# Kernel tuning notes

Hardware: AMD Instinct MI355X
Metric: run time of the kernel (lower is better)

## Reference

```python
import jax, jax.numpy as jnp
import numpy as np

D_MODEL = 256
D_INNER = 512   # expand=2
D_STATE = 16
D_CONV = 4
DT_RANK = 16    # ceil(256/16)
N_LAYERS = 4
CITY = 300
BATCH = 32
EPS = 1e-5


def setup_inputs() -> dict:
    key = jax.random.key(0)
    ks = jax.random.split(key, 12)
    def rn(k, shape, scale=0.02):
        return (jax.random.normal(k, shape) * scale).astype(jnp.float32)
    inp = {}
    inp["coords"]   = jax.random.uniform(ks[0], (BATCH, CITY, 2), jnp.float32)
    inp["emb_W"]    = rn(ks[1], (D_MODEL, 2), 0.5)
    inp["emb_b"]    = jnp.zeros((D_MODEL,), jnp.float32)
    inp["ln_w"]     = jnp.ones((N_LAYERS, D_MODEL), jnp.float32)
    inp["ln_b"]     = jnp.zeros((N_LAYERS, D_MODEL), jnp.float32)
    inp["in_W"]     = rn(ks[2], (N_LAYERS, 2 * D_INNER, D_MODEL))
    inp["conv_W"]   = rn(ks[3], (N_LAYERS, D_INNER, D_CONV), 0.1)
    inp["conv_b"]   = jnp.zeros((N_LAYERS, D_INNER), jnp.float32)
    inp["xproj_W"]  = rn(ks[4], (N_LAYERS, DT_RANK + 2 * D_STATE, D_INNER))
    inp["dtproj_W"] = rn(ks[5], (N_LAYERS, D_INNER, DT_RANK), 0.1)
    inp["dtproj_b"] = rn(ks[6], (N_LAYERS, D_INNER), 0.1)
    # A initialized like mamba: S4D-real, A = -exp(A_log) with A in [1, 16]
    inp["A_log"]    = jnp.log(1.0 + jax.random.uniform(ks[7], (N_LAYERS, D_INNER, D_STATE), jnp.float32) * 15.0)
    inp["D_skip"]   = jnp.ones((N_LAYERS, D_INNER), jnp.float32)
    inp["out_W"]    = rn(ks[8], (N_LAYERS, D_MODEL, D_INNER))
    inp["normf_w"]  = jnp.ones((D_MODEL,), jnp.float32)
    inp["normf_b"]  = jnp.zeros((D_MODEL,), jnp.float32)
    inp["head_W"]   = rn(ks[9], (CITY, D_MODEL))
    return inp


def _layernorm(x, w, b):
    m = jnp.mean(x, axis=-1, keepdims=True)
    v = jnp.mean(jnp.square(x - m), axis=-1, keepdims=True)
    return (x - m) * jax.lax.rsqrt(v + EPS) * w + b


def _mamba_mixer(x, in_W, conv_W, conv_b, xproj_W, dtproj_W, dtproj_b, A_log, D_skip, out_W):
    # x: (B, L, d_model)
    Bsz = x.shape[0]
    xz = jnp.einsum('bld,ed->ble', x, in_W)            # (B, L, 2*d_inner)
    xi, z = jnp.split(xz, 2, axis=-1)                   # each (B, L, d_inner)
    # causal depthwise conv1d along L
    xc = jnp.swapaxes(xi, 1, 2)                         # (B, d_inner, L)
    xc = jax.lax.conv_general_dilated(
        xc, conv_W[:, None, :], (1,), [(D_CONV - 1, 0)],
        feature_group_count=D_INNER, dimension_numbers=('NCH', 'OIH', 'NCH'))
    xc = jax.nn.silu(jnp.swapaxes(xc, 1, 2) + conv_b)   # (B, L, d_inner)
    dbl = jnp.einsum('bld,ed->ble', xc, xproj_W)        # (B, L, dt_rank + 2*d_state)
    dt, Bm, Cm = jnp.split(dbl, [DT_RANK, DT_RANK + D_STATE], axis=-1)
    dt = jax.nn.softplus(jnp.einsum('blr,dr->bld', dt, dtproj_W) + dtproj_b)  # (B, L, d_inner)
    A = -jnp.exp(A_log)                                 # (d_inner, d_state)

    def step(h, inp):
        x_t, dt_t, B_t, C_t = inp                       # (B,dI),(B,dI),(B,dS),(B,dS)
        dA = jnp.exp(dt_t[..., None] * A)               # (B, dI, dS)
        h = dA * h + (dt_t * x_t)[..., None] * B_t[:, None, :]
        y = jnp.einsum('bds,bs->bd', h, C_t)
        return h, y

    h0 = jnp.zeros((Bsz, D_INNER, D_STATE), x.dtype)
    xs = (jnp.swapaxes(xc, 0, 1), jnp.swapaxes(dt, 0, 1),
          jnp.swapaxes(Bm, 0, 1), jnp.swapaxes(Cm, 0, 1))
    _, ys = jax.lax.scan(step, h0, xs)                  # ys: (L, B, d_inner)
    y = jnp.swapaxes(ys, 0, 1) + xc * D_skip
    y = y * jax.nn.silu(z)
    return jnp.einsum('ble,de->bld', y, out_W)          # (B, L, d_model)


def reference(coords, emb_W, emb_b, ln_w, ln_b, in_W, conv_W, conv_b, xproj_W,
              dtproj_W, dtproj_b, A_log, D_skip, out_W, normf_w, normf_b, head_W):
    x = jnp.einsum('blc,dc->bld', coords, emb_W) + emb_b
    residual = None
    for i in range(N_LAYERS):
        residual = x if residual is None else x + residual
        h = _layernorm(residual, ln_w[i], ln_b[i])
        x = _mamba_mixer(h, in_W[i], conv_W[i], conv_b[i], xproj_W[i],
                         dtproj_W[i], dtproj_b[i], A_log[i], D_skip[i], out_W[i])
    res = x + residual
    # final fused add + RMSNorm (is_rms_norm=True with LayerNorm weight/bias)
    rms = res * jax.lax.rsqrt(jnp.mean(res * res, axis=-1, keepdims=True) + EPS)
    out = rms * normf_w + normf_b
    logits = jnp.einsum('bld,cd->blc', out, head_W)     # (B, L, city_count)
    return logits
```

## Files before the change

kernel.cpp:

```cpp
#include <hip/hip_runtime.h>
#include <hip/hip_bf16.h>
#include <math.h>

#define D_MODEL 256
#define D_INNER 512
#define D_STATE 16
#define D_CONV 4
#define DT_RANK 16
#define N_LAYERS 4
#define CITY 300
#define BATCH 32
#define SEQ 300
#define NTOK (BATCH * SEQ)
#define NSEG 15
#define SEGLEN (SEQ / NSEG)

typedef __attribute__((ext_vector_type(8))) short short8v;
typedef __attribute__((ext_vector_type(4))) float f32x4;
typedef __attribute__((ext_vector_type(2))) float f32x2;

#define L2E_F 1.44269504088896340736f
#define LN2_F 0.69314718055994530942f

__device__ __forceinline__ float fexp2(float x) { return __builtin_amdgcn_exp2f(x); }
__device__ __forceinline__ float flog2(float x) { return __builtin_amdgcn_logf(x); }

__device__ __forceinline__ float fast_sig(float x) {
    return __builtin_amdgcn_rcpf(1.f + fexp2(-x * L2E_F));
}

__device__ __forceinline__ float softplus_f(float x) {
    float t = fexp2(-fabsf(x) * L2E_F);
    return fmaxf(x, 0.f) + flog2(1.f + t) * LN2_F;
}

__device__ __forceinline__ unsigned short f2b(float a) {
    __hip_bfloat16 h = __float2bfloat16(a);
    return *reinterpret_cast<unsigned short*>(&h);
}

__device__ __forceinline__ float b2f(unsigned short u) {
    unsigned int x = ((unsigned int)u) << 16;
    return __uint_as_float(x);
}

__device__ __forceinline__ float dtproj8(const float* rb, const f32x2* w2, float dtbv) {
    const f32x2* r2 = (const f32x2*)rb;
    f32x2 a0, a1, a2, a3;
    a0.x = dtbv; a0.y = 0.f;
    a1.x = 0.f; a1.y = 0.f;
    a2 = a1; a3 = a1;
    a0 = __builtin_elementwise_fma(r2[0], w2[0], a0);
    a1 = __builtin_elementwise_fma(r2[1], w2[1], a1);
    a2 = __builtin_elementwise_fma(r2[2], w2[2], a2);
    a3 = __builtin_elementwise_fma(r2[3], w2[3], a3);
    a0 = __builtin_elementwise_fma(r2[4], w2[4], a0);
    a1 = __builtin_elementwise_fma(r2[5], w2[5], a1);
    a2 = __builtin_elementwise_fma(r2[6], w2[6], a2);
    a3 = __builtin_elementwise_fma(r2[7], w2[7], a3);
    f32x2 s = (a0 + a1) + (a2 + a3);
    return s.x + s.y;
}

__global__ void cvt4_kernel(const float* __restrict__ s0, unsigned short* __restrict__ d0, int n0,
                            const float* __restrict__ s1, unsigned short* __restrict__ d1, int n1,
                            const float* __restrict__ s2, unsigned short* __restrict__ d2, int n2,
                            const float* __restrict__ s3, unsigned short* __restrict__ d3, int n3) {
    int stride = gridDim.x * blockDim.x;
    int tid = blockIdx.x * blockDim.x + threadIdx.x;
    for (int i = tid; i < n0 / 4; i += stride) {
        float4 v = ((const float4*)s0)[i];
        ushort4 o; o.x = f2b(v.x); o.y = f2b(v.y); o.z = f2b(v.z); o.w = f2b(v.w);
        ((ushort4*)d0)[i] = o;
    }
    for (int i = tid; i < n1 / 4; i += stride) {
        float4 v = ((const float4*)s1)[i];
        ushort4 o; o.x = f2b(v.x); o.y = f2b(v.y); o.z = f2b(v.z); o.w = f2b(v.w);
        ((ushort4*)d1)[i] = o;
    }
    for (int i = tid; i < n2 / 4; i += stride) {
        float4 v = ((const float4*)s2)[i];
        ushort4 o; o.x = f2b(v.x); o.y = f2b(v.y); o.z = f2b(v.z); o.w = f2b(v.w);
        ((ushort4*)d2)[i] = o;
    }
    for (int i = tid; i < n3 / 4; i += stride) {
        float4 v = ((const float4*)s3)[i];
        ushort4 o; o.x = f2b(v.x); o.y = f2b(v.y); o.z = f2b(v.z); o.w = f2b(v.w);
        ((ushort4*)d3)[i] = o;
    }
}

__global__ void embed_ln_kernel(const float* __restrict__ coords,
                                const float* __restrict__ eW,
                                const float* __restrict__ eb,
                                const float* __restrict__ w,
                                const float* __restrict__ b,
                                float* __restrict__ resid,
                                unsigned short* __restrict__ hb) {
    int t = blockIdx.x, d = threadIdx.x;
    float c0 = coords[t * 2 + 0];
    float c1 = coords[t * 2 + 1];
    float r = c0 * eW[d * 2 + 0] + c1 * eW[d * 2 + 1] + eb[d];
    resid[t * D_MODEL + d] = r;
    float s1 = r, s2 = r * r;
#pragma unroll
    for (int m = 1; m < 64; m <<= 1) {
        s1 += __shfl_xor(s1, m);
        s2 += __shfl_xor(s2, m);
    }
    __shared__ float p1[4], p2[4];
    if ((d & 63) == 0) { p1[d >> 6] = s1; p2[d >> 6] = s2; }
    __syncthreads();
    s1 = (p1[0] + p1[1]) + (p1[2] + p1[3]);
    s2 = (p2[0] + p2[1]) + (p2[2] + p2[3]);
    float mean = s1 * (1.f / D_MODEL);
    float var = s2 * (1.f / D_MODEL) - mean * mean;
    hb[t * D_MODEL + d] = f2b((r - mean) * rsqrtf(var + 1e-5f) * w[d] + b[d]);
}

template <int BM, int BN, bool GN, bool OB>
__global__ __launch_bounds__(256, 2) void gemm_mfma(const unsigned short* __restrict__ A,
                                                    const unsigned short* __restrict__ W,
                                                    void* __restrict__ C, int N, int K) {
    constexpr int TI = BM / 32;
    constexpr int TJ = BN / 32;
    __shared__ short Als[BM * 32];
    __shared__ short Bls[BN * 32];
    const int tid = threadIdx.x;
    const int lane = tid & 63, wid = tid >> 6;
    const int wr = wid >> 1, wc = wid & 1;
    const int t0 = blockIdx.x * BM, n0 = blockIdx.y * BN;
    f32x4 acc[TI][TJ] = {};

    for (int k0 = 0; k0 < K; k0 += 32) {
#pragma unroll
        for (int it = 0; it < BM / 64; ++it) {
            int s = tid + it * 256;
            int m = s >> 2, q = s & 3;
            uint4 p = *(const uint4*)(A + (size_t)(t0 + m) * K + k0 + q * 8);
            *(uint4*)&Als[(((m >> 4) * 4 + q) * 16 + (m & 15)) * 8] = p;
        }
#pragma unroll
        for (int it = 0; it < BN / 64; ++it) {
            int s = tid + it * 256;
            int n = s >> 2, q = s & 3;
            int nrow = n0 + n;
            uint4 p = make_uint4(0u, 0u, 0u, 0u);
            if (!GN || nrow < N)
                p = *(const uint4*)(W + (size_t)nrow * K + k0 + q * 8);
            *(uint4*)&Bls[(((n >> 4) * 4 + q) * 16 + (n & 15)) * 8] = p;
        }
        __syncthreads();
        short8v af[TI], bf[TJ];
#pragma unroll
        for (int i = 0; i < TI; i++)
            af[i] = *(const short8v*)&Als[(wr * TI + i) * 512 + lane * 8];
#pragma unroll
        for (int j = 0; j < TJ; j++)
            bf[j] = *(const short8v*)&Bls[(wc * TJ + j) * 512 + lane * 8];
#pragma unroll
        for (int i = 0; i < TI; i++)
#pragma unroll
            for (int j = 0; j < TJ; j++)
                acc[i][j] = __builtin_amdgcn_mfma_f32_16x16x32_bf16(
                    af[i], bf[j], acc[i][j], 0, 0, 0);
        __syncthreads();
    }
    const int rq = lane >> 4, cn = lane & 15;
#pragma unroll
    for (int i = 0; i < TI; i++) {
        int trow = t0 + wr * (BM / 2) + i * 16 + rq * 4;
#pragma unroll
        for (int j = 0; j < TJ; j++) {
            int ncol = n0 + wc * (BN / 2) + j * 16 + cn;
            if (!GN || ncol < N) {
#pragma unroll
                for (int reg = 0; reg < 4; reg++) {
                    if constexpr (OB)
                        ((unsigned short*)C)[(size_t)(trow + reg) * N + ncol] =
                            f2b(acc[i][j][reg]);
                    else
                        ((float*)C)[(size_t)(trow + reg) * N + ncol] = acc[i][j][reg];
                }
            }
        }
    }
}

__global__ __launch_bounds__(256, 2) void xproj_conv(
    const unsigned short* __restrict__ xzb,
    const float* __restrict__ cW, const float* __restrict__ cb,
    const unsigned short* __restrict__ W,
    unsigned short* __restrict__ xcb, float* __restrict__ dblo) {
    constexpr int TI = 2, TJ = 2;
    const int K = D_INNER, N = 48;
    __shared__ short Als[64 * 32];
    __shared__ short Bls[64 * 32];
    __shared__ float cwL[D_INNER * 4];
    __shared__ float cbL[D_INNER];
    const int tid = threadIdx.x;
    const int lane = tid & 63, wid = tid >> 6;
    const int wr = wid >> 1, wc = wid & 1;
    const int t0 = blockIdx.x * 64;

    for (int i = tid; i < D_INNER; i += 256) {
        ((float4*)cwL)[i] = ((const float4*)cW)[i];
        cbL[i] = cb[i];
    }
    __syncthreads();

    f32x4 acc[TI][TJ] = {};
    const int m = tid >> 2, q = tid & 3;
    const int t = t0 + m;
    const int l = t % SEQ;

    for (int k0 = 0; k0 < K; k0 += 32) {
        {
            const int ch0 = k0 + q * 8;
            const unsigned short* xr = xzb + (size_t)t * 1024 + ch0;
            uint4 u0 = make_uint4(0u, 0u, 0u, 0u), u1 = u0, u2 = u0, u3;
            if (l >= 3) u0 = *(const uint4*)(xr - 3 * 1024);
            if (l >= 2) u1 = *(const uint4*)(xr - 2 * 1024);
            if (l >= 1) u2 = *(const uint4*)(xr - 1 * 1024);
            u3 = *(const uint4*)xr;
            unsigned int ow0, ow1, ow2, ow3;
#pragma unroll
            for (int c2 = 0; c2 < 4; c2++) {
                unsigned int w0 = (c2 == 0) ? u0.x : (c2 == 1) ? u0.y : (c2 == 2) ? u0.z : u0.w;
                unsigned int w1 = (c2 == 0) ? u1.x : (c2 == 1) ? u1.y : (c2 == 2) ? u1.z : u1.w;
                unsigned int w2 = (c2 == 0) ? u2.x : (c2 == 1) ? u2.y : (c2 == 2) ? u2.z : u2.w;
                unsigned int w3 = (c2 == 0) ? u3.x : (c2 == 1) ? u3.y : (c2 == 2) ? u3.z : u3.w;
                int chA = ch0 + c2 * 2, chB = chA + 1;
                float4 wvA = *(const float4*)&cwL[chA * 4];
                float4 wvB = *(const float4*)&cwL[chB * 4];
                float aA = cbL[chA], aB = cbL[chB];
                aA = fmaf(b2f((unsigned short)(w0 & 0xffffu)), wvA.x, aA);
                aB = fmaf(b2f((unsigned short)(w0 >> 16)), wvB.x, aB);
                aA = fmaf(b2f((unsigned short)(w1 & 0xffffu)), wvA.y, aA);
                aB = fmaf(b2f((unsigned short)(w1 >> 16)), wvB.y, aB);
                aA = fmaf(b2f((unsigned short)(w2 & 0xffffu)), wvA.z, aA);
                aB = fmaf(b2f((unsigned short)(w2 >> 16)), wvB.z, aB);
                aA = fmaf(b2f((unsigned short)(w3 & 0xffffu)), wvA.w, aA);
                aB = fmaf(b2f((unsigned short)(w3 >> 16)), wvB.w, aB);
                aA = aA * fast_sig(aA);
                aB = aB * fast_sig(aB);
                unsigned int pk = (unsigned int)f2b(aA) | ((unsigned int)f2b(aB) << 16);
                if (c2 == 0) ow0 = pk; else if (c2 == 1) ow1 = pk; else if (c2 == 2) ow2 = pk; else ow3 = pk;
            }
            uint4 pk4 = make_uint4(ow0, ow1, ow2, ow3);
            *(uint4*)&Als[(((m >> 4) * 4 + q) * 16 + (m & 15)) * 8] = pk4;
            *(uint4*)(xcb + (size_t)t * 512 + ch0) = pk4;
        }
        {
            int n = tid >> 2;
            uint4 p = make_uint4(0u, 0u, 0u, 0u);
            if (n < N) p = *(const uint4*)(W + (size_t)n * K + k0 + q * 8);
            *(uint4*)&Bls[(((n >> 4) * 4 + q) * 16 + (n & 15)) * 8] = p;
        }
        __syncthreads();
        short8v af[TI], bf[TJ];
#pragma unroll
        for (int i = 0; i < TI; i++)
            af[i] = *(const short8v*)&Als[(wr * TI + i) * 512 + lane * 8];
#pragma unroll
        for (int j = 0; j < TJ; j++)
            bf[j] = *(const short8v*)&Bls[(wc * TJ + j) * 512 + lane * 8];
#pragma unroll
        for (int i = 0; i < TI; i++)
#pragma unroll
            for (int j = 0; j < TJ; j++)
                acc[i][j] = __builtin_amdgcn_mfma_f32_16x16x32_bf16(
                    af[i], bf[j], acc[i][j], 0, 0, 0);
        __syncthreads();
    }
    const int rq = lane >> 4, cn = lane & 15;
#pragma unroll
    for (int i = 0; i < TI; i++) {
        int trow = t0 + (wr * TI + i) * 16 + rq * 4;
#pragma unroll
        for (int j = 0; j < TJ; j++) {
            int ncol = wc * 32 + j * 16 + cn;
            if (ncol < N) {
#pragma unroll
                for (int reg = 0; reg < 4; reg++)
                    dblo[(size_t)(trow + reg) * N + ncol] = acc[i][j][reg];
            }
        }
    }
}

template <bool RMS, bool HEAD>
__global__ __launch_bounds__(256, 2) void gemm_out_ln(const unsigned short* __restrict__ A,
                                                      const unsigned short* __restrict__ W,
                                                      float* __restrict__ resid,
                                                      const float* __restrict__ w,
                                                      const float* __restrict__ b,
                                                      unsigned short* __restrict__ hb,
                                                      const unsigned short* __restrict__ hW,
                                                      float* __restrict__ outp) {
    constexpr int TI = 2, TJ = 8;
    const int K = D_INNER;
    __shared__ short Als[64 * 32];
    __shared__ short Bls[256 * 32];
    __shared__ float rs1[2][64], rs2[2][64];
    __shared__ short hN[HEAD ? 64 * 256 : 1];
    const int tid = threadIdx.x;
    const int lane = tid & 63, wid = tid >> 6;
    const int wr = wid >> 1, wc = wid & 1;
    const int t0 = blockIdx.x * 64;
    f32x4 acc[TI][TJ] = {};

    for (int k0 = 0; k0 < K; k0 += 32) {
        {
            int s = tid;
            int m = s >> 2, q = s & 3;
            uint4 p = *(const uint4*)(A + (size_t)(t0 + m) * K + k0 + q * 8);
            *(uint4*)&Als[(((m >> 4) * 4 + q) * 16 + (m & 15)) * 8] = p;
        }
#pragma unroll
        for (int it = 0; it < 4; ++it) {
            int s = tid + it * 256;
            int n = s >> 2, q = s & 3;
            uint4 p = *(const uint4*)(W + (size_t)n * K + k0 + q * 8);
            *(uint4*)&Bls[(((n >> 4) * 4 + q) * 16 + (n & 15)) * 8] = p;
        }
        __syncthreads();
        short8v af[TI], bf[TJ];
#pragma unroll
        for (int i = 0; i < TI; i++)
            af[i] = *(const short8v*)&Als[(wr * TI + i) * 512 + lane * 8];
#pragma unroll
        for (int j = 0; j < TJ; j++)
            bf[j] = *(const short8v*)&Bls[(wc * TJ + j) * 512 + lane * 8];
#pragma unroll
        for (int i = 0; i < TI; i++)
#pragma unroll
            for (int j = 0; j < TJ; j++)
                acc[i][j] = __builtin_amdgcn_mfma_f32_16x16x32_bf16(
                    af[i], bf[j], acc[i][j], 0, 0, 0);
        __syncthreads();
    }
    const int rq = lane >> 4, cn = lane & 15;
    float s1p[TI][4], s2p[TI][4];
#pragma unroll
    for (int i = 0; i < TI; i++) {
        int trow = t0 + wr * 32 + i * 16 + rq * 4;
#pragma unroll
        for (int reg = 0; reg < 4; reg++) { s1p[i][reg] = 0.f; s2p[i][reg] = 0.f; }
#pragma unroll
        for (int j = 0; j < TJ; j++) {
            int c = wc * 128 + j * 16 + cn;
#pragma unroll
            for (int reg = 0; reg < 4; reg++) {
                float rv = acc[i][j][reg] + resid[(size_t)(trow + reg) * D_MODEL + c];
                acc[i][j][reg] = rv;
                s1p[i][reg] += rv;
                s2p[i][reg] = fmaf(rv, rv, s2p[i][reg]);
            }
        }
    }
#pragma unroll
    for (int m = 1; m < 16; m <<= 1) {
#pragma unroll
        for (int i = 0; i < TI; i++)
#pragma unroll
            for (int reg = 0; reg < 4; reg++) {
                s1p[i][reg] += __shfl_xor(s1p[i][reg], m);
                s2p[i][reg] += __shfl_xor(s2p[i][reg], m);
            }
    }
    if (cn == 0) {
#pragma unroll
        for (int i = 0; i < TI; i++)
#pragma unroll
            for (int reg = 0; reg < 4; reg++) {
                int rloc = wr * 32 + i * 16 + rq * 4 + reg;
                rs1[wc][rloc] = s1p[i][reg];
                rs2[wc][rloc] = s2p[i][reg];
            }
    }
    __syncthreads();
    float wv[TJ], bv[TJ];
#pragma unroll
    for (int j = 0; j < TJ; j++) {
        int c = wc * 128 + j * 16 + cn;
        wv[j] = w[c];
        bv[j] = b[c];
    }
#pragma unroll
    for (int i = 0; i < TI; i++) {
        int trow = t0 + wr * 32 + i * 16 + rq * 4;
#pragma unroll
        for (int reg = 0; reg < 4; reg++) {
            int rloc = wr * 32 + i * 16 + rq * 4 + reg;
            float S1 = rs1[0][rloc] + rs1[1][rloc];
            float S2 = rs2[0][rloc] + rs2[1][rloc];
            float mean, rstd;
            if constexpr (RMS) {
                mean = 0.f;
                rstd = rsqrtf(S2 * (1.f / D_MODEL) + 1e-5f);
            } else {
                mean = S1 * (1.f / D_MODEL);
                float var = S2 * (1.f / D_MODEL) - mean * mean;
                rstd = rsqrtf(var + 1e-5f);
            }
#pragma unroll
            for (int j = 0; j < TJ; j++) {
                int c = wc * 128 + j * 16 + cn;
                float rv = acc[i][j][reg];
                unsigned short nv = f2b((rv - mean) * rstd * wv[j] + bv[j]);
                if constexpr (HEAD) {
                    int mrow = wr * 32 + i * 16 + rq * 4 + reg;
                    hN[(c >> 5) * 2048 + (((mrow >> 4) * 4 + ((c & 31) >> 3)) * 16 + (mrow & 15)) * 8 + (c & 7)] = (short)nv;
                } else {
                    hb[(size_t)(trow + reg) * D_MODEL + c] = nv;
                }
                if constexpr (!RMS)
                    resid[(size_t)(trow + reg) * D_MODEL + c] = rv;
            }
        }
    }
    if constexpr (HEAD) {
        __syncthreads();
        for (int nch = 0; nch < 5; ++nch) {
            f32x4 acc2[2][2] = {};
            for (int k0 = 0; k0 < D_MODEL; k0 += 32) {
                int n = tid >> 2, q = tid & 3;
                int nrow = nch * 64 + n;
                uint4 p = make_uint4(0u, 0u, 0u, 0u);
                if (nrow < CITY) p = *(const uint4*)(hW + (size_t)nrow * D_MODEL + k0 + q * 8);
                *(uint4*)&Bls[(((n >> 4) * 4 + q) * 16 + (n & 15)) * 8] = p;
                __syncthreads();
                short8v af2[2], bf2[2];
#pragma unroll
                for (int i = 0; i < 2; i++)
                    af2[i] = *(const short8v*)&hN[(k0 >> 5) * 2048 + (wr * 2 + i) * 512 + lane * 8];
#pragma unroll
                for (int j = 0; j < 2; j++)
                    bf2[j] = *(const short8v*)&Bls[(wc * 2 + j) * 512 + lane * 8];
#pragma unroll
                for (int i = 0; i < 2; i++)
#pragma unroll
                    for (int j = 0; j < 2; j++)
                        acc2[i][j] = __builtin_amdgcn_mfma_f32_16x16x32_bf16(
                            af2[i], bf2[j], acc2[i][j], 0, 0, 0);
                __syncthreads();
            }
#pragma unroll
            for (int i = 0; i < 2; i++) {
                int trow = t0 + (wr * 2 + i) * 16 + rq * 4;
#pragma unroll
                for (int j = 0; j < 2; j++) {
                    int ncol = nch * 64 + wc * 32 + j * 16 + cn;
                    if (ncol < CITY) {
#pragma unroll
                        for (int reg = 0; reg < 4; reg++)
                            outp[(size_t)(trow + reg) * CITY + ncol] = acc2[i][j][reg];
                    }
                }
            }
        }
    }
}

__global__ __launch_bounds__(960) void scan_block(
    const unsigned short* __restrict__ xcb, const float* __restrict__ dbl,
    const unsigned short* __restrict__ xzb,
    const float* __restrict__ A_log, const float* __restrict__ Dskip,
    const float* __restrict__ dtW, const float* __restrict__ dtb,
    float* __restrict__ dts, unsigned short* __restrict__ yb) {
    __shared__ float lh[NSEG * D_STATE * 64];
    __shared__ float lsd[NSEG * 64];
    const int b = blockIdx.x, dg = blockIdx.y;
    const int tid = threadIdx.x;
    const int lane = tid & 63;
    const int seg = __builtin_amdgcn_readfirstlane(tid >> 6);
    const int d = (dg << 6) + lane;
    f32x2 A2[8], w2[8];
#pragma unroll
    for (int s4 = 0; s4 < 4; s4++) {
        float4 v = *(const float4*)(A_log + (size_t)d * D_STATE + s4 * 4);
        f32x2 pa, pb;
        pa.x = -fexp2(v.x * L2E_F) * L2E_F;
        pa.y = -fexp2(v.y * L2E_F) * L2E_F;
        pb.x = -fexp2(v.z * L2E_F) * L2E_F;
        pb.y = -fexp2(v.w * L2E_F) * L2E_F;
        A2[s4 * 2 + 0] = pa;
        A2[s4 * 2 + 1] = pb;
        float4 w = *(const float4*)(dtW + (size_t)d * DT_RANK + s4 * 4);
        f32x2 qa, qb;
        qa.x = w.x; qa.y = w.y;
        qb.x = w.z; qb.y = w.w;
        w2[s4 * 2 + 0] = qa;
        w2[s4 * 2 + 1] = qb;
    }
    const float dtbv = dtb[d], dsk = Dskip[d];
    const size_t tb = (size_t)b * SEQ + (size_t)seg * SEGLEN;
    const float* __restrict__ dr = dbl + tb * 48;
    const unsigned short* __restrict__ xp = xcb + tb * 512 + d;
    const unsigned short* __restrict__ zp = xzb + tb * 1024 + 512 + d;
    float* __restrict__ dtp = dts + tb * 512 + d;
    unsigned short* __restrict__ yp = yb + tb * 512 + d;

    {
        f32x2 h2[8];
#pragma unroll
        for (int i = 0; i < 8; i++) { h2[i].x = 0.f; h2[i].y = 0.f; }
        float sdt = 0.f;
        float dbA[32], dbB[32];
#pragma unroll
        for (int i = 0; i < 8; i++) ((float4*)dbA)[i] = ((const float4*)dr)[i];
        float xv = b2f(xp[0]);
        for (int l = 0; l < SEGLEN; l += 2) {
            const float4* nr1 = (const float4*)(dr + (size_t)(l + 1) * 48);
#pragma unroll
            for (int i = 0; i < 8; i++) ((float4*)dbB)[i] = nr1[i];
            float xv1 = b2f(xp[(size_t)(l + 1) * 512]);
            {
                float acc = dtproj8(dbA, w2, dtbv);
                float dtt = softplus_f(acc);
                dtp[(size_t)l * 512] = dtt;
                sdt += dtt;
                float dtx = dtt * xv;
                f32x2 dtt2, dtx2;
                dtt2.x = dtt; dtt2.y = dtt;
                dtx2.x = dtx; dtx2.y = dtx;
                const f32x2* B2 = (const f32x2*)(dbA + 16);
#pragma unroll
                for (int i = 0; i < 8; i++) {
                    f32x2 g = dtt2 * A2[i];
                    f32x2 e;
                    e.x = fexp2(g.x);
                    e.y = fexp2(g.y);
                    h2[i] = __builtin_elementwise_fma(e, h2[i], dtx2 * B2[i]);
                }
            }
            const float4* nr2 = (const float4*)(dr + (size_t)(l + 2) * 48);
#pragma unroll
            for (int i = 0; i < 8; i++) ((float4*)dbA)[i] = nr2[i];
            float xv2 = b2f(xp[(size_t)(l + 2) * 512]);
            if (l + 1 < SEGLEN) {
                float acc = dtproj8(dbB, w2, dtbv);
                float dtt = softplus_f(acc);
                dtp[(size_t)(l + 1) * 512] = dtt;
                sdt += dtt;
                float dtx = dtt * xv1;
                f32x2 dtt2, dtx2;
                dtt2.x = dtt; dtt2.y = dtt;
                dtx2.x = dtx; dtx2.y = dtx;
                const f32x2* B2 = (const f32x2*)(dbB + 16);
#pragma unroll
                for (int i = 0; i < 8; i++) {
                    f32x2 g = dtt2 * A2[i];
                    f32x2 e;
                    e.x = fexp2(g.x);
                    e.y = fexp2(g.y);
                    h2[i] = __builtin_elementwise_fma(e, h2[i], dtx2 * B2[i]);
                }
            }
            xv = xv2;
        }
#pragma unroll
        for (int i = 0; i < 8; i++) {
            lh[(seg * D_STATE + 2 * i + 0) * 64 + lane] = h2[i].x;
            lh[(seg * D_STATE + 2 * i + 1) * 64 + lane] = h2[i].y;
        }
        lsd[seg * 64 + lane] = sdt;
    }
    __syncthreads();
    for (int it = tid; it < D_STATE * 64; it += 960) {
        int ch = it & 63, s = it >> 6;
        float As2 = -fexp2(A_log[(size_t)((dg << 6) + ch) * D_STATE + s] * L2E_F) * L2E_F;
        float hl[NSEG], sd[NSEG];
#pragma unroll
        for (int sg = 0; sg < NSEG; sg++) {
            hl[sg] = lh[(sg * D_STATE + s) * 64 + ch];
            sd[sg] = lsd[sg * 64 + ch];
        }
        float H = 0.f;
#pragma unroll
        for (int sg = 0; sg < NSEG; sg++) {
            lh[(sg * D_STATE + s) * 64 + ch] = H;
            H = fmaf(fexp2(As2 * sd[sg]), H, hl[sg]);
        }
    }
    __syncthreads();
    {
        f32x2 h2[8];
#pragma unroll
        for (int i = 0; i < 8; i++) {
            h2[i].x = lh[(seg * D_STATE + 2 * i + 0) * 64 + lane];
            h2[i].y = lh[(seg * D_STATE + 2 * i + 1) * 64 + lane];
        }
        float dbA[32], dbB[32];
#pragma unroll
        for (int i = 0; i < 8; i++) ((float4*)dbA)[i] = ((const float4*)(dr + 16))[i];
        float xv = b2f(xp[0]), zv = b2f(zp[0]);
        float dt0 = dtp[0];
        for (int l = 0; l < SEGLEN; l += 2) {
            const float4* nr1 = (const float4*)(dr + (size_t)(l + 1) * 48 + 16);
#pragma unroll
            for (int i = 0; i < 8; i++) ((float4*)dbB)[i] = nr1[i];
            float xv1 = b2f(xp[(size_t)(l + 1) * 512]);
            float zv1 = b2f(zp[(size_t)(l + 1) * 1024]);
            float dt1 = dtp[(size_t)(l + 1) * 512];
            {
                float dtt = dt0;
                float dtx = dtt * xv;
                f32x2 dtt2, dtx2;
                dtt2.x = dtt; dtt2.y = dtt;
                dtx2.x = dtx; dtx2.y = dtx;
                f32x2 ya, yc;
                ya.x = 0.f; ya.y = 0.f; yc = ya;
                const f32x2* B2 = (const f32x2*)dbA;
                const f32x2* C2 = (const f32x2*)(dbA + 16);
#pragma unroll
                for (int i = 0; i < 8; i++) {
                    f32x2 g = dtt2 * A2[i];
                    f32x2 e;
                    e.x = fexp2(g.x);
                    e.y = fexp2(g.y);
                    h2[i] = __builtin_elementwise_fma(e, h2[i], dtx2 * B2[i]);
                    if (i & 1)
                        yc = __builtin_elementwise_fma(h2[i], C2[i], yc);
                    else
                        ya = __builtin_elementwise_fma(h2[i], C2[i], ya);
                }
                f32x2 ys = ya + yc;
                float y = ys.x + ys.y;
                yp[(size_t)l * 512] = f2b((y + xv * dsk) * (zv * fast_sig(zv)));
            }
            const float4* nr2 = (const float4*)(dr + (size_t)(l + 2) * 48 + 16);
#pragma unroll
            for (int i = 0; i < 8; i++) ((float4*)dbA)[i] = nr2[i];
            float xv2 = b2f(xp[(size_t)(l + 2) * 512]);
            float zv2 = b2f(zp[(size_t)(l + 2) * 1024]);
            float dt2 = dtp[(size_t)(l + 2) * 512];
            if (l + 1 < SEGLEN) {
                float dtt = dt1;
                float dtx = dtt * xv1;
                f32x2 dtt2, dtx2;
                dtt2.x = dtt; dtt2.y = dtt;
                dtx2.x = dtx; dtx2.y = dtx;
                f32x2 ya, yc;
                ya.x = 0.f; ya.y = 0.f; yc = ya;
                const f32x2* B2 = (const f32x2*)dbB;
                const f32x2* C2 = (const f32x2*)(dbB + 16);
#pragma unroll
                for (int i = 0; i < 8; i++) {
                    f32x2 g = dtt2 * A2[i];
                    f32x2 e;
                    e.x = fexp2(g.x);
                    e.y = fexp2(g.y);
                    h2[i] = __builtin_elementwise_fma(e, h2[i], dtx2 * B2[i]);
                    if (i & 1)
                        yc = __builtin_elementwise_fma(h2[i], C2[i], yc);
                    else
                        ya = __builtin_elementwise_fma(h2[i], C2[i], ya);
                }
                f32x2 ys = ya + yc;
                float y = ys.x + ys.y;
                yp[(size_t)(l + 1) * 512] = f2b((y + xv1 * dsk) * (zv1 * fast_sig(zv1)));
            }
            xv = xv2; zv = zv2; dt0 = dt2;
        }
    }
}

extern "C" void kernel_launch(void* const* d_in, const int* in_sizes, int n_in,
                              void* d_out, int out_size, void* d_ws, size_t ws_size,
                              hipStream_t stream) {
    const float* coords   = (const float*)d_in[0];
    const float* emb_W    = (const float*)d_in[1];
    const float* emb_b    = (const float*)d_in[2];
    const float* ln_w     = (const float*)d_in[3];
    const float* ln_b     = (const float*)d_in[4];
    const float* in_W     = (const float*)d_in[5];
    const float* conv_W   = (const float*)d_in[6];
    const float* conv_b   = (const float*)d_in[7];
    const float* xproj_W  = (const float*)d_in[8];
    const float* dtproj_W = (const float*)d_in[9];
    const float* dtproj_b = (const float*)d_in[10];
    const float* A_log    = (const float*)d_in[11];
    const float* D_skip   = (const float*)d_in[12];
    const float* out_W    = (const float*)d_in[13];
    const float* normf_w  = (const float*)d_in[14];
    const float* normf_b  = (const float*)d_in[15];
    const float* head_W   = (const float*)d_in[16];
    float* out = (float*)d_out;

    const int T = NTOK;
    float* resid = (float*)d_ws;
    float* dbl   = resid + (size_t)T * D_MODEL;
    float* dts   = dbl + (size_t)T * 48;
    unsigned short* hb     = (unsigned short*)(dts + (size_t)T * D_INNER);
    unsigned short* xzb    = hb + (size_t)T * D_MODEL;
    unsigned short* xcb    = xzb + (size_t)T * 2 * D_INNER;
    unsigned short* yb     = xcb + (size_t)T * D_INNER;
    unsigned short* wb_in  = yb + (size_t)T * D_INNER;
    unsigned short* wb_xp  = wb_in + (size_t)N_LAYERS * 2 * D_INNER * D_MODEL;
    unsigned short* wb_out = wb_xp + (size_t)N_LAYERS * 48 * D_INNER;
    unsigned short* wb_hd  = wb_out + (size_t)N_LAYERS * D_MODEL * D_INNER;

    cvt4_kernel<<<256, 256, 0, stream>>>(
        in_W, wb_in, N_LAYERS * 2 * D_INNER * D_MODEL,
        xproj_W, wb_xp, N_LAYERS * 48 * D_INNER,
        out_W, wb_out, N_LAYERS * D_MODEL * D_INNER,
        head_W, wb_hd, CITY * D_MODEL);

    embed_ln_kernel<<<T, D_MODEL, 0, stream>>>(coords, emb_W, emb_b, ln_w, ln_b, resid, hb);

    for (int i = 0; i < N_LAYERS; i++) {
        gemm_mfma<128, 128, false, true><<<dim3(T / 128, 8), 256, 0, stream>>>(
            hb, wb_in + (size_t)i * 2 * D_INNER * D_MODEL, xzb, 2 * D_INNER, D_MODEL);
        xproj_conv<<<T / 64, 256, 0, stream>>>(
            xzb, conv_W + i * D_INNER * D_CONV, conv_b + i * D_INNER,
            wb_xp + (size_t)i * 48 * D_INNER, xcb, dbl);
        scan_block<<<dim3(BATCH, 8), 960, 0, stream>>>(
            xcb, dbl, xzb, A_log + (size_t)i * D_INNER * D_STATE, D_skip + i * D_INNER,
            dtproj_W + (size_t)i * D_INNER * DT_RANK, dtproj_b + i * D_INNER, dts, yb);
        if (i < N_LAYERS - 1)
            gemm_out_ln<false, false><<<T / 64, 256, 0, stream>>>(
                yb, wb_out + (size_t)i * D_MODEL * D_INNER, resid,
                ln_w + (i + 1) * D_MODEL, ln_b + (i + 1) * D_MODEL, hb, nullptr, nullptr);
        else
            gemm_out_ln<true, true><<<T / 64, 256, 0, stream>>>(
                yb, wb_out + (size_t)i * D_MODEL * D_INNER, resid,
                normf_w, normf_b, hb, wb_hd, out);
    }
}
```

Baseline: 463.2 us.

## Compute local scan output in first pass, correct with carried-in state in second

The chunked scan now computes the full local output (zero-initial-state contribution plus D skip) during the first pass and writes it to a new fp32 workspace buffer. The second pass then only propagates the carried-in prefix state, which decays by exp(dt*A) and is dotted with C, then adds it to the stored partial before gating. This removes the B*x update and dt/x reloads from the second pass, shortening the work after the segment-combine barrier. In exchange it adds an extra fp32 write and read per element and more register pressure from 48-float row buffers in the first pass.

```diff
diff --git a/kernel.cpp b/kernel.cpp
--- a/kernel.cpp
+++ b/kernel.cpp
@@ -468,7 +468,8 @@
     const unsigned short* __restrict__ xzb,
     const float* __restrict__ A_log, const float* __restrict__ Dskip,
     const float* __restrict__ dtW, const float* __restrict__ dtb,
-    float* __restrict__ dts, unsigned short* __restrict__ yb) {
+    float* __restrict__ dts, float* __restrict__ wls,
+    unsigned short* __restrict__ yb) {
     __shared__ float lh[NSEG * D_STATE * 64];
     __shared__ float lsd[NSEG * 64];
     const int b = blockIdx.x, dg = blockIdx.y;
@@ -500,6 +501,7 @@
     const unsigned short* __restrict__ xp = xcb + tb * 512 + d;
     const unsigned short* __restrict__ zp = xzb + tb * 1024 + 512 + d;
     float* __restrict__ dtp = dts + tb * 512 + d;
+    float* __restrict__ wlp = wls + tb * 512 + d;
     unsigned short* __restrict__ yp = yb + tb * 512 + d;
 
     {
@@ -507,14 +509,14 @@
 #pragma unroll
         for (int i = 0; i < 8; i++) { h2[i].x = 0.f; h2[i].y = 0.f; }
         float sdt = 0.f;
-        float dbA[32], dbB[32];
-#pragma unroll
-        for (int i = 0; i < 8; i++) ((float4*)dbA)[i] = ((const float4*)dr)[i];
+        float dbA[48], dbB[48];
+#pragma unroll
+        for (int i = 0; i < 12; i++) ((float4*)dbA)[i] = ((const float4*)dr)[i];
         float xv = b2f(xp[0]);
         for (int l = 0; l < SEGLEN; l += 2) {
             const float4* nr1 = (const float4*)(dr + (size_t)(l + 1) * 48);
 #pragma unroll
-            for (int i = 0; i < 8; i++) ((float4*)dbB)[i] = nr1[i];
+            for (int i = 0; i < 12; i++) ((float4*)dbB)[i] = nr1[i];
             float xv1 = b2f(xp[(size_t)(l + 1) * 512]);
             {
                 float acc = dtproj8(dbA, w2, dtbv);
@@ -526,94 +528,9 @@
                 dtt2.x = dtt; dtt2.y = dtt;
                 dtx2.x = dtx; dtx2.y = dtx;
                 const f32x2* B2 = (const f32x2*)(dbA + 16);
-#pragma unroll
-                for (int i = 0; i < 8; i++) {
-                    f32x2 g = dtt2 * A2[i];
-                    f32x2 e;
-                    e.x = fexp2(g.x);
-                    e.y = fexp2(g.y);
-                    h2[i] = __builtin_elementwise_fma(e, h2[i], dtx2 * B2[i]);
-                }
-            }
-            const float4* nr2 = (const float4*)(dr + (size_t)(l + 2) * 48);
-#pragma unroll
-            for (int i = 0; i < 8; i++) ((float4*)dbA)[i] = nr2[i];
-            float xv2 = b2f(xp[(size_t)(l + 2) * 512]);
-            if (l + 1 < SEGLEN) {
-                float acc = dtproj8(dbB, w2, dtbv);
-                float dtt = softplus_f(acc);
-                dtp[(size_t)(l + 1) * 512] = dtt;
-                sdt += dtt;
-                float dtx = dtt * xv1;
-                f32x2 dtt2, dtx2;
-                dtt2.x = dtt; dtt2.y = dtt;
-                dtx2.x = dtx; dtx2.y = dtx;
-                const f32x2* B2 = (const f32x2*)(dbB + 16);
-#pragma unroll
-                for (int i = 0; i < 8; i++) {
-                    f32x2 g = dtt2 * A2[i];
-                    f32x2 e;
-                    e.x = fexp2(g.x);
-                    e.y = fexp2(g.y);
-                    h2[i] = __builtin_elementwise_fma(e, h2[i], dtx2 * B2[i]);
-                }
-            }
-            xv = xv2;
-        }
-#pragma unroll
-        for (int i = 0; i < 8; i++) {
-            lh[(seg * D_STATE + 2 * i + 0) * 64 + lane] = h2[i].x;
-            lh[(seg * D_STATE + 2 * i + 1) * 64 + lane] = h2[i].y;
-        }
-        lsd[seg * 64 + lane] = sdt;
-    }
-    __syncthreads();
-    for (int it = tid; it < D_STATE * 64; it += 960) {
-        int ch = it & 63, s = it >> 6;
-        float As2 = -fexp2(A_log[(size_t)((dg << 6) + ch) * D_STATE + s] * L2E_F) * L2E_F;
-        float hl[NSEG], sd[NSEG];
-#pragma unroll
-        for (int sg = 0; sg < NSEG; sg++) {
-            hl[sg] = lh[(sg * D_STATE + s) * 64 + ch];
-            sd[sg] = lsd[sg * 64 + ch];
-        }
-        float H = 0.f;
-#pragma unroll
-        for (int sg = 0; sg < NSEG; sg++) {
-            lh[(sg * D_STATE + s) * 64 + ch] = H;
-            H = fmaf(fexp2(As2 * sd[sg]), H, hl[sg]);
-        }
-    }
-    __syncthreads();
-    {
-        f32x2 h2[8];
-#pragma unroll
-        for (int i = 0; i < 8; i++) {
-            h2[i].x = lh[(seg * D_STATE + 2 * i + 0) * 64 + lane];
-            h2[i].y = lh[(seg * D_STATE + 2 * i + 1) * 64 + lane];
-        }
-        float dbA[32], dbB[32];
-#pragma unroll
-        for (int i = 0; i < 8; i++) ((float4*)dbA)[i] = ((const float4*)(dr + 16))[i];
-        float xv = b2f(xp[0]), zv = b2f(zp[0]);
-        float dt0 = dtp[0];
-        for (int l = 0; l < SEGLEN; l += 2) {
-            const float4* nr1 = (const float4*)(dr + (size_t)(l + 1) * 48 + 16);
-#pragma unroll
-            for (int i = 0; i < 8; i++) ((float4*)dbB)[i] = nr1[i];
-            float xv1 = b2f(xp[(size_t)(l + 1) * 512]);
-            float zv1 = b2f(zp[(size_t)(l + 1) * 1024]);
-            float dt1 = dtp[(size_t)(l + 1) * 512];
-            {
-                float dtt = dt0;
-                float dtx = dtt * xv;
-                f32x2 dtt2, dtx2;
-                dtt2.x = dtt; dtt2.y = dtt;
-                dtx2.x = dtx; dtx2.y = dtx;
+                const f32x2* C2 = (const f32x2*)(dbA + 32);
                 f32x2 ya, yc;
                 ya.x = 0.f; ya.y = 0.f; yc = ya;
-                const f32x2* B2 = (const f32x2*)dbA;
-                const f32x2* C2 = (const f32x2*)(dbA + 16);
 #pragma unroll
                 for (int i = 0; i < 8; i++) {
                     f32x2 g = dtt2 * A2[i];
@@ -627,25 +544,25 @@
                         ya = __builtin_elementwise_fma(h2[i], C2[i], ya);
                 }
                 f32x2 ys = ya + yc;
-                float y = ys.x + ys.y;
-                yp[(size_t)l * 512] = f2b((y + xv * dsk) * (zv * fast_sig(zv)));
-            }
-            const float4* nr2 = (const float4*)(dr + (size_t)(l + 2) * 48 + 16);
-#pragma unroll
-            for (int i = 0; i < 8; i++) ((float4*)dbA)[i] = nr2[i];
+                wlp[(size_t)l * 512] = (ys.x + ys.y) + xv * dsk;
+            }
+            const float4* nr2 = (const float4*)(dr + (size_t)(l + 2) * 48);
+#pragma unroll
+            for (int i = 0; i < 12; i++) ((float4*)dbA)[i] = nr2[i];
             float xv2 = b2f(xp[(size_t)(l + 2) * 512]);
-            float zv2 = b2f(zp[(size_t)(l + 2) * 1024]);
-            float dt2 = dtp[(size_t)(l + 2) * 512];
             if (l + 1 < SEGLEN) {
-                float dtt = dt1;
+                float acc = dtproj8(dbB, w2, dtbv);
+                float dtt = softplus_f(acc);
+                dtp[(size_t)(l + 1) * 512] = dtt;
+                sdt += dtt;
                 float dtx = dtt * xv1;
                 f32x2 dtt2, dtx2;
                 dtt2.x = dtt; dtt2.y = dtt;
                 dtx2.x = dtx; dtx2.y = dtx;
+                const f32x2* B2 = (const f32x2*)(dbB + 16);
+                const f32x2* C2 = (const f32x2*)(dbB + 32);
                 f32x2 ya, yc;
                 ya.x = 0.f; ya.y = 0.f; yc = ya;
-                const f32x2* B2 = (const f32x2*)dbB;
-                const f32x2* C2 = (const f32x2*)(dbB + 16);
 #pragma unroll
                 for (int i = 0; i < 8; i++) {
                     f32x2 g = dtt2 * A2[i];
@@ -659,10 +576,108 @@
                         ya = __builtin_elementwise_fma(h2[i], C2[i], ya);
                 }
                 f32x2 ys = ya + yc;
-                float y = ys.x + ys.y;
-                yp[(size_t)(l + 1) * 512] = f2b((y + xv1 * dsk) * (zv1 * fast_sig(zv1)));
-            }
-            xv = xv2; zv = zv2; dt0 = dt2;
+                wlp[(size_t)(l + 1) * 512] = (ys.x + ys.y) + xv1 * dsk;
+            }
+            xv = xv2;
+        }
+#pragma unroll
+        for (int i = 0; i < 8; i++) {
+            lh[(seg * D_STATE + 2 * i + 0) * 64 + lane] = h2[i].x;
+            lh[(seg * D_STATE + 2 * i + 1) * 64 + lane] = h2[i].y;
+        }
+        lsd[seg * 64 + lane] = sdt;
+    }
+    __syncthreads();
+    for (int it = tid; it < D_STATE * 64; it += 960) {
+        int ch = it & 63, s = it >> 6;
+        float As2 = -fexp2(A_log[(size_t)((dg << 6) + ch) * D_STATE + s] * L2E_F) * L2E_F;
+        float hl[NSEG], sd[NSEG];
+#pragma unroll
+        for (int sg = 0; sg < NSEG; sg++) {
+            hl[sg] = lh[(sg * D_STATE + s) * 64 + ch];
+            sd[sg] = lsd[sg * 64 + ch];
+        }
+        float H = 0.f;
+#pragma unroll
+        for (int sg = 0; sg < NSEG; sg++) {
+            lh[(sg * D_STATE + s) * 64 + ch] = H;
+            H = fmaf(fexp2(As2 * sd[sg]), H, hl[sg]);
+        }
+    }
+    __syncthreads();
+    {
+        f32x2 hc[8];
+#pragma unroll
+        for (int i = 0; i < 8; i++) {
+            hc[i].x = lh[(seg * D_STATE + 2 * i + 0) * 64 + lane];
+            hc[i].y = lh[(seg * D_STATE + 2 * i + 1) * 64 + lane];
+        }
+        float cbA[16], cbB[16];
+#pragma unroll
+        for (int i = 0; i < 4; i++) ((float4*)cbA)[i] = ((const float4*)(dr + 32))[i];
+        float zv = b2f(zp[0]);
+        float dt0 = dtp[0];
+        float wl0 = wlp[0];
+        for (int l = 0; l < SEGLEN; l += 2) {
+            const float4* nr1 = (const float4*)(dr + (size_t)(l + 1) * 48 + 32);
+#pragma unroll
+            for (int i = 0; i < 4; i++) ((float4*)cbB)[i] = nr1[i];
+            float zv1 = b2f(zp[(size_t)(l + 1) * 1024]);
+            float dt1 = dtp[(size_t)(l + 1) * 512];
+            float wl1 = wlp[(size_t)(l + 1) * 512];
+            {
+                float dtt = dt0;
+                f32x2 dtt2;
+                dtt2.x = dtt; dtt2.y = dtt;
+                const f32x2* C2 = (const f32x2*)cbA;
+                f32x2 ya, yc;
+                ya.x = 0.f; ya.y = 0.f; yc = ya;
+#pragma unroll
+                for (int i = 0; i < 8; i++) {
+                    f32x2 g = dtt2 * A2[i];
+                    f32x2 e;
+                    e.x = fexp2(g.x);
+                    e.y = fexp2(g.y);
+                    hc[i] = hc[i] * e;
+                    if (i & 1)
+                        yc = __builtin_elementwise_fma(hc[i], C2[i], yc);
+                    else
+                        ya = __builtin_elementwise_fma(hc[i], C2[i], ya);
+                }
+                f32x2 ys = ya + yc;
+                float y = wl0 + (ys.x + ys.y);
+                yp[(size_t)l * 512] = f2b(y * (zv * fast_sig(zv)));
+            }
+            const float4* nr2 = (const float4*)(dr + (size_t)(l + 2) * 48 + 32);
+#pragma unroll
+            for (int i = 0; i < 4; i++) ((float4*)cbA)[i] = nr2[i];
+            float zv2 = b2f(zp[(size_t)(l + 2) * 1024]);
+            float dt2 = dtp[(size_t)(l + 2) * 512];
+            float wl2 = wlp[(size_t)(l + 2) * 512];
+            if (l + 1 < SEGLEN) {
+                float dtt = dt1;
+                f32x2 dtt2;
+                dtt2.x = dtt; dtt2.y = dtt;
+                const f32x2* C2 = (const f32x2*)cbB;
+                f32x2 ya, yc;
+                ya.x = 0.f; ya.y = 0.f; yc = ya;
+#pragma unroll
+                for (int i = 0; i < 8; i++) {
+                    f32x2 g = dtt2 * A2[i];
+                    f32x2 e;
+                    e.x = fexp2(g.x);
+                    e.y = fexp2(g.y);
+                    hc[i] = hc[i] * e;
+                    if (i & 1)
+                        yc = __builtin_elementwise_fma(hc[i], C2[i], yc);
+                    else
+                        ya = __builtin_elementwise_fma(hc[i], C2[i], ya);
+                }
+                f32x2 ys = ya + yc;
+                float y = wl1 + (ys.x + ys.y);
+                yp[(size_t)(l + 1) * 512] = f2b(y * (zv1 * fast_sig(zv1)));
+            }
+            zv = zv2; dt0 = dt2; wl0 = wl2;
         }
     }
 }
@@ -693,7 +708,8 @@
     float* resid = (float*)d_ws;
     float* dbl   = resid + (size_t)T * D_MODEL;
     float* dts   = dbl + (size_t)T * 48;
-    unsigned short* hb     = (unsigned short*)(dts + (size_t)T * D_INNER);
+    float* wls   = dts + (size_t)T * D_INNER;
+    unsigned short* hb     = (unsigned short*)(wls + (size_t)T * D_INNER);
     unsigned short* xzb    = hb + (size_t)T * D_MODEL;
     unsigned short* xcb    = xzb + (size_t)T * 2 * D_INNER;
     unsigned short* yb     = xcb + (size_t)T * D_INNER;
@@ -718,7 +734,7 @@
             wb_xp + (size_t)i * 48 * D_INNER, xcb, dbl);
         scan_block<<<dim3(BATCH, 8), 960, 0, stream>>>(
             xcb, dbl, xzb, A_log + (size_t)i * D_INNER * D_STATE, D_skip + i * D_INNER,
-            dtproj_W + (size_t)i * D_INNER * DT_RANK, dtproj_b + i * D_INNER, dts, yb);
+            dtproj_W + (size_t)i * D_INNER * DT_RANK, dtproj_b + i * D_INNER, dts, wls, yb);
         if (i < N_LAYERS - 1)
             gemm_out_ln<false, false><<<T / 64, 256, 0, stream>>>(
                 yb, wb_out + (size_t)i * D_MODEL * D_INNER, resid,
```

Measured after the change: 467.0 us. About the same (+0.8%).
